# Performance work log

Measured on AMD Instinct MI355X. Metric: run time of the kernel, lower is better.

## Reference

```python
import jax, jax.numpy as jnp
import numpy as np

N, D, H, DH, E = 4096, 256, 4, 64, 131072  # nodes, embed dim, heads, head dim, edges
ALPHA = 0.2  # LeakyReLU negative slope
NEG = -9.0e15  # mask fill value from the torch code (-9000000000000000.0)


def setup_inputs() -> dict:
    key = jax.random.key(0)
    ks = jax.random.split(key, 10)
    x = jax.random.normal(ks[0], (N, D), dtype=jnp.float32)
    edge_index = jax.random.randint(ks[1], (2, E), 0, N, dtype=jnp.int32)
    edge_vals = jax.random.uniform(ks[2], (E,), dtype=jnp.float32)
    # EdgeWeightAttention MLP: Linear(2D -> D), ReLU, Linear(D -> 1)
    W1 = jax.random.normal(ks[3], (2 * D, D), dtype=jnp.float32) * (1.0 / np.sqrt(2 * D))
    b1 = jnp.zeros((D,), dtype=jnp.float32)
    W2 = jax.random.normal(ks[4], (D, 1), dtype=jnp.float32) * (1.0 / np.sqrt(D))
    b2 = jnp.zeros((1,), dtype=jnp.float32)
    # Per-head GAT params (stacked over heads): W [H, D, DH], a_src/a_dst [H, DH]
    gain = 1.414
    W = jax.random.normal(ks[5], (H, D, DH), dtype=jnp.float32) * (gain * np.sqrt(2.0 / (D + DH)))
    a_src = jax.random.normal(ks[6], (H, DH), dtype=jnp.float32) * (gain * np.sqrt(2.0 / (1 + DH)))
    a_dst = jax.random.normal(ks[7], (H, DH), dtype=jnp.float32) * (gain * np.sqrt(2.0 / (1 + DH)))
    return {"x": x, "edge_vals": edge_vals, "W1": W1, "b1": b1, "W2": W2, "b2": b2,
            "W": W, "a_src": a_src, "a_dst": a_dst, "edge_index": edge_index}


def reference(x, edge_vals, W1, b1, W2, b2, W, a_src, a_dst, edge_index):
    n = x.shape[0]
    row, col = edge_index[0], edge_index[1]
    # --- EdgeWeightAttention: gather endpoint features, tiny MLP + sigmoid, rescale edge values ---
    ef = jnp.concatenate([x[row], x[col]], axis=1)                       # [E, 2D]
    aw = jax.nn.sigmoid(jax.nn.relu(ef @ W1 + b1) @ W2 + b2)[:, 0]       # [E]
    new_vals = edge_vals * aw                                            # [E]
    # Densify reweighted sparse adj (values are positive -> used only as mask adj>0 in GAT)
    adj = jnp.zeros((n, n), dtype=x.dtype).at[row, col].set(new_vals)    # [N, N]
    # --- Multi-head GAT, vectorized over heads ---
    h = jnp.einsum('nd,hde->hne', x, W)                                  # [H, N, DH]
    esrc = jnp.einsum('hne,he->hn', h, a_src)                            # [H, N]
    edst = jnp.einsum('hne,he->hn', h, a_dst)                            # [H, N]
    e = jax.nn.leaky_relu(esrc[:, :, None] + edst[:, None, :], ALPHA)    # [H, N, N]
    e = jnp.where(adj[None, :, :] > 0, e, jnp.asarray(NEG, x.dtype))
    attn = jax.nn.softmax(e, axis=-1)                                    # [H, N, N]
    out = jnp.einsum('hij,hje->hie', attn, h)                            # [H, N, DH]
    return jnp.transpose(out, (1, 0, 2)).reshape(n, H * DH)              # [N, D]
```

## Files before the change

### kernel.cpp

```cpp
#include <hip/hip_runtime.h>
#include <hip/hip_bf16.h>

#define NN    4096
#define DD    256
#define HH    4
#define DHH   64
#define EDGES 131072
#define CAP   128
#define RPB   2
#define LRELU_ALPHA 0.2f

typedef __hip_bfloat16 bf16;
typedef __attribute__((ext_vector_type(8))) short short8v;
typedef __attribute__((ext_vector_type(4))) float f32x4;


__device__ __forceinline__ float bf_lo(unsigned int u) { return __uint_as_float(u << 16); }
__device__ __forceinline__ float bf_hi(unsigned int u) { return __uint_as_float(u & 0xffff0000u); }

__device__ __forceinline__ unsigned short f2bf_rne(float f) {
    unsigned int u = __float_as_uint(f);
    return (unsigned short)((u + 0x7fffu + ((u >> 16) & 1u)) >> 16);
}
__device__ __forceinline__ float bf2f(unsigned short s) {
    return __uint_as_float(((unsigned int)s) << 16);
}

__global__ __launch_bounds__(1024) void hproj_edges_kernel(
    const float* __restrict__ x, const float* __restrict__ W,
    const float* __restrict__ a_src, const float* __restrict__ a_dst,
    const int* __restrict__ ei, const float* __restrict__ ev,
    bf16* __restrict__ hb, float* __restrict__ esrc, float* __restrict__ edst,
    unsigned int* __restrict__ bmg)
{
    __shared__ float pvs[16][16];
    __shared__ float pvd[16][16];

    const int t  = threadIdx.x;
    const int i0 = blockIdx.x * 16;

    if (t < 512) {
        const int   e  = blockIdx.x * 512 + t;
        const float vv = ev[e];
        const int   er = ei[e];
        const int   ec = ei[EDGES + e];
        if (vv > 0.f)
            atomicOr(&bmg[er * (NN / 32) + (ec >> 5)], 1u << (ec & 31));
    }

    const int wv   = t >> 6;
    const int h    = wv >> 2;
    const int q    = wv & 3;
    const int lane = t & 63;
    const int mrow = lane & 15;
    const int kgrp = lane >> 4;

    const float* xp = x + (size_t)(i0 + mrow) * DD + 8 * kgrp;
    const float* Wb = W + (size_t)h * (DD * DHH) + q * 16 + mrow;

    f32x4 acc = (f32x4){0.f, 0.f, 0.f, 0.f};

    #pragma unroll
    for (int ks = 0; ks < 8; ++ks) {
        const float4 u0 = *(const float4*)(xp + ks * 32);
        const float4 u1 = *(const float4*)(xp + ks * 32 + 4);
        const float v[8] = {u0.x, u0.y, u0.z, u0.w, u1.x, u1.y, u1.z, u1.w};
        short8v ah, al;
        #pragma unroll
        for (int e = 0; e < 8; ++e) {
            const unsigned short hi = f2bf_rne(v[e]);
            ah[e] = (short)hi;
            al[e] = (short)f2bf_rne(v[e] - bf2f(hi));
        }
        const float* wk = Wb + (size_t)(ks * 32 + 8 * kgrp) * DHH;
        short8v bh, bl;
        #pragma unroll
        for (int e = 0; e < 8; ++e) {
            const float we = wk[(size_t)e * DHH];
            const unsigned short hi = f2bf_rne(we);
            bh[e] = (short)hi;
            bl[e] = (short)f2bf_rne(we - bf2f(hi));
        }
        acc = __builtin_amdgcn_mfma_f32_16x16x32_bf16(ah, bh, acc, 0, 0, 0);
        acc = __builtin_amdgcn_mfma_f32_16x16x32_bf16(ah, bl, acc, 0, 0, 0);
        acc = __builtin_amdgcn_mfma_f32_16x16x32_bf16(al, bh, acc, 0, 0, 0);
    }

    {
        const int col = h * 64 + q * 16 + mrow;
        #pragma unroll
        for (int reg = 0; reg < 4; ++reg) {
            const int row = i0 + 4 * kgrp + reg;
            hb[(size_t)row * (HH * DHH) + col] = __float2bfloat16(acc[reg]);
        }
    }

    {
        const float as = a_src[h * DHH + q * 16 + mrow];
        const float ad = a_dst[h * DHH + q * 16 + mrow];
        float vs[4], vd[4];
        #pragma unroll
        for (int reg = 0; reg < 4; ++reg) {
            vs[reg] = acc[reg] * as;
            vd[reg] = acc[reg] * ad;
        }
        #pragma unroll
        for (int reg = 0; reg < 4; ++reg) {
            #pragma unroll
            for (int off = 1; off < 16; off <<= 1) {
                vs[reg] += __shfl_xor(vs[reg], off, 64);
                vd[reg] += __shfl_xor(vd[reg], off, 64);
            }
        }
        if (mrow == 0) {
            #pragma unroll
            for (int reg = 0; reg < 4; ++reg) {
                pvs[wv][4 * kgrp + reg] = vs[reg];
                pvd[wv][4 * kgrp + reg] = vd[reg];
            }
        }
    }
    __syncthreads();

    if (q == 0 && lane < 16) {
        float s = 0.f, d = 0.f;
        #pragma unroll
        for (int qq = 0; qq < 4; ++qq) {
            s += pvs[h * 4 + qq][lane];
            d += pvd[h * 4 + qq][lane];
        }
        esrc[(i0 + lane) * HH + h] = s;
        edst[(i0 + lane) * HH + h] = d;
    }
}

__global__ __launch_bounds__(128) void attn_kernel(
    const unsigned int* __restrict__ bmg, const bf16* __restrict__ hb,
    const float* __restrict__ esrc, const float* __restrict__ edst,
    float* __restrict__ out)
{
    __shared__ int nbr[RPB][CAP];
    __shared__ __align__(16) float wts[RPB][CAP][HH];

    const int t = threadIdx.x;
    const int r = t >> 6, lane = t & 63;
    const int i = blockIdx.x * RPB + r;

    const uint2 wp = *(const uint2*)(bmg + (size_t)i * (NN / 32) + 2 * lane);
    const int c = __popc(wp.x) + __popc(wp.y);
    int inc = c;
    #pragma unroll
    for (int off = 1; off < 64; off <<= 1) {
        const int nn = __shfl_up(inc, off, 64);
        if (lane >= off) inc += nn;
    }
    int p = inc - c;
    const int deg = min(__shfl(inc, 63, 64), CAP);
    unsigned int w = wp.x;
    while (w) { const int b = __ffs(w) - 1; w &= w - 1; if (p < CAP) nbr[r][p] = (lane << 6) + b; ++p; }
    w = wp.y;
    while (w) { const int b = __ffs(w) - 1; w &= w - 1; if (p < CAP) nbr[r][p] = (lane << 6) + 32 + b; ++p; }
    __syncthreads();

    const int head = lane >> 4;
    float4 acc = make_float4(0.f, 0.f, 0.f, 0.f);
    float4 sm  = make_float4(0.f, 0.f, 0.f, 0.f);

    if (deg > 0) {
        const float4 es4 = *(const float4*)(esrc + (size_t)i * HH);
        float4 mx = make_float4(-INFINITY, -INFINITY, -INFINITY, -INFINITY);
        for (int k = lane; k < deg; k += 64) {
            const float4 ed = *(const float4*)(edst + (size_t)nbr[r][k] * HH);
            float4 e4;
            e4.x = es4.x + ed.x; e4.x = e4.x > 0.f ? e4.x : LRELU_ALPHA * e4.x;
            e4.y = es4.y + ed.y; e4.y = e4.y > 0.f ? e4.y : LRELU_ALPHA * e4.y;
            e4.z = es4.z + ed.z; e4.z = e4.z > 0.f ? e4.z : LRELU_ALPHA * e4.z;
            e4.w = es4.w + ed.w; e4.w = e4.w > 0.f ? e4.w : LRELU_ALPHA * e4.w;
            *(float4*)&wts[r][k][0] = e4;
            mx.x = fmaxf(mx.x, e4.x); mx.y = fmaxf(mx.y, e4.y);
            mx.z = fmaxf(mx.z, e4.z); mx.w = fmaxf(mx.w, e4.w);
        }
        #pragma unroll
        for (int off = 32; off; off >>= 1) {
            mx.x = fmaxf(mx.x, __shfl_xor(mx.x, off, 64));
            mx.y = fmaxf(mx.y, __shfl_xor(mx.y, off, 64));
            mx.z = fmaxf(mx.z, __shfl_xor(mx.z, off, 64));
            mx.w = fmaxf(mx.w, __shfl_xor(mx.w, off, 64));
        }
        for (int k = lane; k < deg; k += 64) {
            float4 e4 = *(const float4*)&wts[r][k][0];
            e4.x = expf(e4.x - mx.x); e4.y = expf(e4.y - mx.y);
            e4.z = expf(e4.z - mx.z); e4.w = expf(e4.w - mx.w);
            *(float4*)&wts[r][k][0] = e4;
            sm.x += e4.x; sm.y += e4.y; sm.z += e4.z; sm.w += e4.w;
        }
        #pragma unroll
        for (int off = 32; off; off >>= 1) {
            sm.x += __shfl_xor(sm.x, off, 64);
            sm.y += __shfl_xor(sm.y, off, 64);
            sm.z += __shfl_xor(sm.z, off, 64);
            sm.w += __shfl_xor(sm.w, off, 64);
        }
    }
    __syncthreads();

    float inv;
    if (deg == 0) {
        const uint2* hp = (const uint2*)hb + lane;
        for (int j = 0; j < NN; ++j) {
            const uint2 u = hp[(size_t)j * 64];
            acc.x += bf_lo(u.x); acc.y += bf_hi(u.x);
            acc.z += bf_lo(u.y); acc.w += bf_hi(u.y);
        }
        inv = 1.f / NN;
    } else {
        const uint2* hp = (const uint2*)hb;
        int k = 0;
        for (; k + 3 < deg; k += 4) {
            const int j0 = nbr[r][k],     j1 = nbr[r][k + 1];
            const int j2 = nbr[r][k + 2], j3 = nbr[r][k + 3];
            const uint2 u0 = hp[(size_t)j0 * 64 + lane];
            const uint2 u1 = hp[(size_t)j1 * 64 + lane];
            const uint2 u2 = hp[(size_t)j2 * 64 + lane];
            const uint2 u3 = hp[(size_t)j3 * 64 + lane];
            const float w0 = wts[r][k][head],     w1 = wts[r][k + 1][head];
            const float w2 = wts[r][k + 2][head], w3 = wts[r][k + 3][head];
            acc.x = fmaf(w0, bf_lo(u0.x), acc.x); acc.y = fmaf(w0, bf_hi(u0.x), acc.y);
            acc.z = fmaf(w0, bf_lo(u0.y), acc.z); acc.w = fmaf(w0, bf_hi(u0.y), acc.w);
            acc.x = fmaf(w1, bf_lo(u1.x), acc.x); acc.y = fmaf(w1, bf_hi(u1.x), acc.y);
            acc.z = fmaf(w1, bf_lo(u1.y), acc.z); acc.w = fmaf(w1, bf_hi(u1.y), acc.w);
            acc.x = fmaf(w2, bf_lo(u2.x), acc.x); acc.y = fmaf(w2, bf_hi(u2.x), acc.y);
            acc.z = fmaf(w2, bf_lo(u2.y), acc.z); acc.w = fmaf(w2, bf_hi(u2.y), acc.w);
            acc.x = fmaf(w3, bf_lo(u3.x), acc.x); acc.y = fmaf(w3, bf_hi(u3.x), acc.y);
            acc.z = fmaf(w3, bf_lo(u3.y), acc.z); acc.w = fmaf(w3, bf_hi(u3.y), acc.w);
        }
        for (; k < deg; ++k) {
            const uint2 u = hp[(size_t)nbr[r][k] * 64 + lane];
            const float wk = wts[r][k][head];
            acc.x = fmaf(wk, bf_lo(u.x), acc.x); acc.y = fmaf(wk, bf_hi(u.x), acc.y);
            acc.z = fmaf(wk, bf_lo(u.y), acc.z); acc.w = fmaf(wk, bf_hi(u.y), acc.w);
        }
        const float s = head == 0 ? sm.x : head == 1 ? sm.y : head == 2 ? sm.z : sm.w;
        inv = 1.f / s;
    }

    float4 o;
    o.x = acc.x * inv; o.y = acc.y * inv; o.z = acc.z * inv; o.w = acc.w * inv;
    *(float4*)(out + (size_t)i * (HH * DHH) + 4 * lane) = o;
}

extern "C" void kernel_launch(void* const* d_in, const int* in_sizes, int n_in,
                              void* d_out, int out_size, void* d_ws, size_t ws_size,
                              hipStream_t stream)
{
    const float* x     = (const float*)d_in[0];
    const float* ev    = (const float*)d_in[1];
    const float* W     = (const float*)d_in[6];
    const float* a_src = (const float*)d_in[7];
    const float* a_dst = (const float*)d_in[8];
    const int*   ei    = (const int*)d_in[9];
    float* out = (float*)d_out;

    char* ws = (char*)d_ws;
    bf16*  hb    = (bf16*)ws;
    float* esrc  = (float*)(ws + 2097152);
    float* edst  = (float*)(ws + 2162688);
    unsigned int* bmg = (unsigned int*)(ws + 2228224);

    hipMemsetAsync(bmg, 0, NN * (NN / 32) * sizeof(unsigned int), stream);
    hproj_edges_kernel<<<NN / 16, 1024, 0, stream>>>(x, W, a_src, a_dst, ei, ev,
                                                     hb, esrc, edst, bmg);
    attn_kernel<<<NN / RPB, 128, 0, stream>>>(bmg, hb, esrc, edst, out);
}
```

Before: 102.8 us.

## Stage per-head W split into bf16 hi/lo in LDS, remap blocks to head x 64 rows

Each block now handles one head and 64 rows instead of all heads for 16 rows. It converts that head's W slice once into bf16 hi/lo pairs stored in shared memory, laid out so each lane reads its MFMA B-fragment with four 32-bit loads. The aim is to remove the repeated strided global W reads and per-warp bf16 splitting in the inner loop. The cost is about 80KB of LDS per block, which limits occupancy, plus a sync-guarded staging prologue.

```diff
diff --git a/kernel.cpp b/kernel.cpp
--- a/kernel.cpp
+++ b/kernel.cpp
@@ -33,14 +33,18 @@
     bf16* __restrict__ hb, float* __restrict__ esrc, float* __restrict__ edst,
     unsigned int* __restrict__ bmg)
 {
+    __shared__ unsigned short wlhi[2048 * 10];
+    __shared__ unsigned short wllo[2048 * 10];
     __shared__ float pvs[16][16];
     __shared__ float pvd[16][16];
 
-    const int t  = threadIdx.x;
-    const int i0 = blockIdx.x * 16;
+    const int t   = threadIdx.x;
+    const int blk = blockIdx.x;
+    const int h   = blk & 3;
+    const int i0  = (blk >> 2) * 64;
 
     if (t < 512) {
-        const int   e  = blockIdx.x * 512 + t;
+        const int   e  = blk * 512 + t;
         const float vv = ev[e];
         const int   er = ei[e];
         const int   ec = ei[EDGES + e];
@@ -48,15 +52,38 @@
             atomicOr(&bmg[er * (NN / 32) + (ec >> 5)], 1u << (ec & 31));
     }
 
+    {
+        const float4* Ws = (const float4*)(W + (size_t)h * (DD * DHH));
+        #pragma unroll
+        for (int j = 0; j < 4; ++j) {
+            const int fi = t + j * 1024;
+            const float4 f = Ws[fi];
+            const float v[4] = {f.x, f.y, f.z, f.w};
+            #pragma unroll
+            for (int c = 0; c < 4; ++c) {
+                const int lin = fi * 4 + c;
+                const int d = lin >> 6, dh = lin & 63;
+                const int rec = (((dh >> 4) * 8 + (d >> 5)) << 6)
+                              + ((d >> 3) & 3) * 16 + (dh & 15);
+                const int off = rec * 10 + (d & 7);
+                const unsigned short hi = f2bf_rne(v[c]);
+                wlhi[off] = hi;
+                wllo[off] = f2bf_rne(v[c] - bf2f(hi));
+            }
+        }
+    }
+    __syncthreads();
+
     const int wv   = t >> 6;
-    const int h    = wv >> 2;
+    const int m    = wv >> 2;
     const int q    = wv & 3;
     const int lane = t & 63;
     const int mrow = lane & 15;
     const int kgrp = lane >> 4;
 
-    const float* xp = x + (size_t)(i0 + mrow) * DD + 8 * kgrp;
-    const float* Wb = W + (size_t)h * (DD * DHH) + q * 16 + mrow;
+    const float* xp = x + (size_t)(i0 + m * 16 + mrow) * DD + 8 * kgrp;
+    const unsigned int* hi32 = (const unsigned int*)wlhi;
+    const unsigned int* lo32 = (const unsigned int*)wllo;
 
     f32x4 acc = (f32x4){0.f, 0.f, 0.f, 0.f};
 
@@ -72,25 +99,23 @@
             ah[e] = (short)hi;
             al[e] = (short)f2bf_rne(v[e] - bf2f(hi));
         }
-        const float* wk = Wb + (size_t)(ks * 32 + 8 * kgrp) * DHH;
-        short8v bh, bl;
-        #pragma unroll
-        for (int e = 0; e < 8; ++e) {
-            const float we = wk[(size_t)e * DHH];
-            const unsigned short hi = f2bf_rne(we);
-            bh[e] = (short)hi;
-            bl[e] = (short)f2bf_rne(we - bf2f(hi));
-        }
-        acc = __builtin_amdgcn_mfma_f32_16x16x32_bf16(ah, bh, acc, 0, 0, 0);
-        acc = __builtin_amdgcn_mfma_f32_16x16x32_bf16(ah, bl, acc, 0, 0, 0);
-        acc = __builtin_amdgcn_mfma_f32_16x16x32_bf16(al, bh, acc, 0, 0, 0);
+        const int rb = ((q * 8 + ks) * 64 + lane) * 5;
+        union { unsigned int u[4]; short8v s; } bh, bl;
+        #pragma unroll
+        for (int k = 0; k < 4; ++k) {
+            bh.u[k] = hi32[rb + k];
+            bl.u[k] = lo32[rb + k];
+        }
+        acc = __builtin_amdgcn_mfma_f32_16x16x32_bf16(ah, bh.s, acc, 0, 0, 0);
+        acc = __builtin_amdgcn_mfma_f32_16x16x32_bf16(ah, bl.s, acc, 0, 0, 0);
+        acc = __builtin_amdgcn_mfma_f32_16x16x32_bf16(al, bh.s, acc, 0, 0, 0);
     }
 
     {
         const int col = h * 64 + q * 16 + mrow;
         #pragma unroll
         for (int reg = 0; reg < 4; ++reg) {
-            const int row = i0 + 4 * kgrp + reg;
+            const int row = i0 + m * 16 + 4 * kgrp + reg;
             hb[(size_t)row * (HH * DHH) + col] = __float2bfloat16(acc[reg]);
         }
     }
@@ -126,11 +151,12 @@
         float s = 0.f, d = 0.f;
         #pragma unroll
         for (int qq = 0; qq < 4; ++qq) {
-            s += pvs[h * 4 + qq][lane];
-            d += pvd[h * 4 + qq][lane];
-        }
-        esrc[(i0 + lane) * HH + h] = s;
-        edst[(i0 + lane) * HH + h] = d;
+            s += pvs[m * 4 + qq][lane];
+            d += pvd[m * 4 + qq][lane];
+        }
+        const int row = i0 + m * 16 + lane;
+        esrc[row * HH + h] = s;
+        edst[row * HH + h] = d;
     }
 }
 
@@ -268,7 +294,7 @@
     unsigned int* bmg = (unsigned int*)(ws + 2228224);
 
     hipMemsetAsync(bmg, 0, NN * (NN / 32) * sizeof(unsigned int), stream);
-    hproj_edges_kernel<<<NN / 16, 1024, 0, stream>>>(x, W, a_src, a_dst, ei, ev,
-                                                     hb, esrc, edst, bmg);
+    hproj_edges_kernel<<<256, 1024, 0, stream>>>(x, W, a_src, a_dst, ei, ev,
+                                                 hb, esrc, edst, bmg);
     attn_kernel<<<NN / RPB, 128, 0, stream>>>(bmg, hb, esrc, edst, out);
 }
```

Measured after the change: 102.9 us. No clear change (+0.0%).
